# Performance work log

Measured on AMD Instinct MI355X. Metric: run time of the kernel, lower is better.

## Reference

```python
import jax, jax.numpy as jnp
import numpy as np

N_NODES = 100000
N_EDGES = 1000000
IN_DIM = 128
HID1 = 64
HID2 = 64
OUT_DIM = 1
NUM_GRAPHS = 2048


def setup_inputs() -> dict:
    key = jax.random.key(0)
    ks = jax.random.split(key, 12)
    x = jax.random.normal(ks[0], (N_NODES, IN_DIM), dtype=jnp.float32)
    edge_index = jax.random.randint(ks[1], (2, N_EDGES), 0, N_NODES, dtype=jnp.int64)
    batch = jnp.sort(jax.random.randint(ks[2], (N_NODES,), 0, NUM_GRAPHS, dtype=jnp.int64))
    s1 = 1.0 / np.sqrt(IN_DIM)
    s2 = 1.0 / np.sqrt(HID1)
    s3 = 1.0 / np.sqrt(HID2)
    return {
        "x": x,
        "edge_index": edge_index,
        "batch": batch,
        "W1": jax.random.normal(ks[3], (IN_DIM, HID1), dtype=jnp.float32) * s1,
        "b1": jnp.zeros((HID1,), dtype=jnp.float32),
        "W2": jax.random.normal(ks[4], (HID1, HID2), dtype=jnp.float32) * s2,
        "b2": jnp.zeros((HID2,), dtype=jnp.float32),
        "attn_w": jax.random.normal(ks[5], (HID2, 1), dtype=jnp.float32) * s3,
        "attn_b": jnp.zeros((1,), dtype=jnp.float32),
        "mask_w": jax.random.normal(ks[6], (HID2, 1), dtype=jnp.float32) * s3,
        "mask_b": jnp.zeros((1,), dtype=jnp.float32),
        "out_w": jax.random.normal(ks[7], (HID2, OUT_DIM), dtype=jnp.float32) * s3,
        "out_b": jnp.zeros((OUT_DIM,), dtype=jnp.float32),
    }


def reference(x, edge_index, batch, W1, b1, W2, b2, attn_w, attn_b, mask_w, mask_b, out_w, out_b):
    n = x.shape[0]
    # GCNConv (PyG default): add self-loops, symmetric normalization
    loop = jnp.arange(n, dtype=edge_index.dtype)
    row = jnp.concatenate([edge_index[0], loop])  # source nodes
    col = jnp.concatenate([edge_index[1], loop])  # target nodes
    deg = jax.ops.segment_sum(jnp.ones_like(col, dtype=x.dtype), col, num_segments=n)
    dinv = jnp.where(deg > 0, jax.lax.rsqrt(jnp.maximum(deg, 1e-12)), 0.0)
    norm = dinv[row] * dinv[col]  # [E+N]

    def conv(h, W, b):
        h = h @ W                              # [N, out]
        m = h[row] * norm[:, None]             # gather + scale  [E+N, out]
        return jax.ops.segment_sum(m, col, num_segments=n) + b

    h = jax.nn.relu(conv(x, W1, b1))
    h = jax.nn.relu(conv(h, W2, b2))
    # AttentionPooling: (attn score * sigmoid mask)-weighted scatter-sum per graph
    scores = (h @ attn_w + attn_b) * jax.nn.sigmoid(h @ mask_w + mask_b)  # [N,1]
    pooled = jax.ops.segment_sum(h * scores, batch, num_segments=NUM_GRAPHS)  # [G, HID2]
    return pooled @ out_w + out_b
```

## Files before the change

### kernel.cpp

```cpp
#include <hip/hip_runtime.h>
#include <math.h>


#define NB 64
#define SEG 16
#define CAPS 80
#define SLOTS (SEG * CAPS)
#define BIN_BLOCKS 256

__global__ __launch_bounds__(256) void gemm_bin_kernel(
    const float* __restrict__ X, const float* __restrict__ W,
    float* __restrict__ P, int N, int K,
    const int* __restrict__ row, const int* __restrict__ col,
    int* __restrict__ bcnt, int* __restrict__ gbuf, int E,
    float* __restrict__ out, const float* __restrict__ out_b, int G) {
    __shared__ float Wl[32 * 64];
    __shared__ float xs[32 * 132];

    if (blockIdx.x < BIN_BLOCKS) {
        int seg = blockIdx.x & (SEG - 1);
        int t = blockIdx.x * 256 + threadIdx.x;
        if (t < G) out[t] = out_b[0];
        for (int e = t; e < E; e += BIN_BLOCKS * 256) {
            int c = col[e];
            int b = c >> 6;
            int pos = atomicAdd(&bcnt[(b * SEG + seg) * 16], 1);
            if (pos < CAPS) gbuf[b * SLOTS + seg * CAPS + pos] = row[e] | ((c & 63) << 17);
        }
        return;
    }

    const int tid = threadIdx.x;
    const int cg = tid & 7;
    const int ng = tid >> 3;
    const int node0 = (blockIdx.x - BIN_BLOCKS) * 128;

    float acc[4][8];
#pragma unroll
    for (int r = 0; r < 4; r++)
#pragma unroll
        for (int j = 0; j < 8; j++) acc[r][j] = 0.0f;

    for (int k0 = 0; k0 < K; k0 += 32) {
        const float4* Wg = (const float4*)(W + (size_t)k0 * 64);
#pragma unroll
        for (int f = tid; f < 512; f += 256) ((float4*)Wl)[f] = Wg[f];
        {
            int rrow = tid >> 1;
            int q0 = (tid & 1) * 16;
            int node = node0 + rrow;
            const float* Xr = X + (size_t)node * K + k0 + q0;
#pragma unroll
            for (int q = 0; q < 4; q++) {
                float4 v = make_float4(0.f, 0.f, 0.f, 0.f);
                if (node < N) v = *(const float4*)(Xr + 4 * q);
                int kb = q0 + 4 * q;
                xs[(kb + 0) * 132 + rrow] = v.x;
                xs[(kb + 1) * 132 + rrow] = v.y;
                xs[(kb + 2) * 132 + rrow] = v.z;
                xs[(kb + 3) * 132 + rrow] = v.w;
            }
        }
        __syncthreads();
#pragma unroll
        for (int kk = 0; kk < 32; kk++) {
            float4 xv = *(const float4*)&xs[kk * 132 + ng * 4];
            const float* wr = &Wl[kk * 64 + cg * 8];
            float4 w0 = *(const float4*)(wr + 0);
            float4 w1 = *(const float4*)(wr + 4);
#pragma unroll
            for (int r = 0; r < 4; r++) {
                float xr = (r == 0) ? xv.x : (r == 1) ? xv.y : (r == 2) ? xv.z : xv.w;
                acc[r][0] = fmaf(xr, w0.x, acc[r][0]);
                acc[r][1] = fmaf(xr, w0.y, acc[r][1]);
                acc[r][2] = fmaf(xr, w0.z, acc[r][2]);
                acc[r][3] = fmaf(xr, w0.w, acc[r][3]);
                acc[r][4] = fmaf(xr, w1.x, acc[r][4]);
                acc[r][5] = fmaf(xr, w1.y, acc[r][5]);
                acc[r][6] = fmaf(xr, w1.z, acc[r][6]);
                acc[r][7] = fmaf(xr, w1.w, acc[r][7]);
            }
        }
        __syncthreads();
    }

#pragma unroll
    for (int r = 0; r < 4; r++) {
        int node = node0 + ng * 4 + r;
        if (node < N) {
            float* dst = P + (size_t)node * 64 + cg * 8;
            *(float4*)(dst + 0) = make_float4(acc[r][0], acc[r][1], acc[r][2], acc[r][3]);
            *(float4*)(dst + 4) = make_float4(acc[r][4], acc[r][5], acc[r][6], acc[r][7]);
        }
    }
}

__global__ __launch_bounds__(256) void sort_kernel(
    const int* __restrict__ bcnt, const int* __restrict__ gbuf,
    int* __restrict__ csr, int* __restrict__ startcnt,
    float* __restrict__ dinv, float* __restrict__ P, int N) {
    __shared__ int scnt[SEG], segoff[SEG], s_tot;
    __shared__ int ebuf[SLOTS];
    __shared__ int lcnt[NB], lcur[NB];
    __shared__ float sdinv[NB];
    const int tid = threadIdx.x;
    const int b = blockIdx.x;
    const int base = b * SLOTS;

    if (tid < SEG) {
        int c = bcnt[(b * SEG + tid) * 16];
        scnt[tid] = c < CAPS ? c : CAPS;
    }
    if (tid < NB) lcnt[tid] = 0;
    __syncthreads();
    if (tid == 0) {
        int o = 0;
        for (int s = 0; s < SEG; s++) { segoff[s] = o; o += scnt[s]; }
        s_tot = o;
    }
    __syncthreads();
    for (int idx = tid; idx < SLOTS; idx += 256) {
        int seg = idx / CAPS;
        int j = idx - seg * CAPS;
        if (j < scnt[seg]) {
            int w = gbuf[base + idx];
            ebuf[segoff[seg] + j] = w;
            atomicAdd(&lcnt[(w >> 17) & 63], 1);
        }
    }
    __syncthreads();
    if (tid < NB) {
        int cntv = lcnt[tid];
        int rnd = (cntv + 3) & ~3;
        int val = rnd;
#pragma unroll
        for (int off = 1; off < 64; off <<= 1) {
            int n = __shfl_up(val, off, 64);
            if (tid >= off) val += n;
        }
        int st = val - rnd;
        lcur[tid] = st;
        float d = rsqrtf(1.0f + (float)cntv);
        sdinv[tid] = d;
        int v = b * NB + tid;
        if (v < N) {
            dinv[v] = d;
            int cc = cntv < 127 ? cntv : 127;
            startcnt[v] = ((base + st) << 7) | cc;
        }
    }
    __syncthreads();
    int tot = s_tot;
    for (int idx = tid; idx < tot; idx += 256) {
        int w = ebuf[idx];
        int vl = (w >> 17) & 63;
        int pp = atomicAdd(&lcur[vl], 1);
        csr[base + pp] = w & 131071;
    }
    for (int idx = tid; idx < NB * 16; idx += 256) {
        int r = idx >> 4;
        int v = b * NB + r;
        if (v < N) {
            float d = sdinv[r];
            float4* pp = (float4*)(P + (size_t)v * 64) + (idx & 15);
            float4 t = *pp;
            t.x *= d; t.y *= d; t.z *= d; t.w *= d;
            *pp = t;
        }
    }
}

__global__ __launch_bounds__(256) void gather_gemm_kernel(
    const float* __restrict__ P, const int* __restrict__ csr,
    const int* __restrict__ startcnt, const float* __restrict__ dinv,
    const float* __restrict__ b1, const float* __restrict__ W2,
    float* __restrict__ Q, int N) {
    __shared__ float hs[64 * 65];
    __shared__ float Wl[64 * 64];
    const int tid = threadIdx.x;
    const int v0 = blockIdx.x * 64;
    const int vend = (v0 + 64 < N) ? v0 + 64 : N;
    const int p = tid & 15;
    const int p4 = p * 4;

    for (int f = tid; f < 1024; f += 256)
        ((float4*)Wl)[f] = ((const float4*)W2)[f];

    const float4 bb = ((const float4*)b1)[p];
    for (int v = v0 + (tid >> 4); v < vend; v += 16) {
        int pack = startcnt[v];
        int st = pack >> 7;
        int c = pack & 127;
        float dv = dinv[v];
        float4 acc = *(const float4*)(P + (size_t)v * 64 + p4);
        for (int i = 0; i < c; i += 8) {
            int4 ua = *(const int4*)(csr + st + i);
            int4 ub = *(const int4*)(csr + st + i + 4);
            float4 m0 = *(const float4*)(P + (size_t)ua.x * 64 + p4);
            float4 m1 = *(const float4*)(P + (size_t)ua.y * 64 + p4);
            float4 m2 = *(const float4*)(P + (size_t)ua.z * 64 + p4);
            float4 m3 = *(const float4*)(P + (size_t)ua.w * 64 + p4);
            float4 m4 = *(const float4*)(P + (size_t)ub.x * 64 + p4);
            float4 m5 = *(const float4*)(P + (size_t)ub.y * 64 + p4);
            float4 m6 = *(const float4*)(P + (size_t)ub.z * 64 + p4);
            float4 m7 = *(const float4*)(P + (size_t)ub.w * 64 + p4);
            acc.x += m0.x; acc.y += m0.y; acc.z += m0.z; acc.w += m0.w;
            if (i + 1 < c) { acc.x += m1.x; acc.y += m1.y; acc.z += m1.z; acc.w += m1.w; }
            if (i + 2 < c) { acc.x += m2.x; acc.y += m2.y; acc.z += m2.z; acc.w += m2.w; }
            if (i + 3 < c) { acc.x += m3.x; acc.y += m3.y; acc.z += m3.z; acc.w += m3.w; }
            if (i + 4 < c) { acc.x += m4.x; acc.y += m4.y; acc.z += m4.z; acc.w += m4.w; }
            if (i + 5 < c) { acc.x += m5.x; acc.y += m5.y; acc.z += m5.z; acc.w += m5.w; }
            if (i + 6 < c) { acc.x += m6.x; acc.y += m6.y; acc.z += m6.z; acc.w += m6.w; }
            if (i + 7 < c) { acc.x += m7.x; acc.y += m7.y; acc.z += m7.z; acc.w += m7.w; }
        }
        float* hd = &hs[(v - v0) * 65 + p4];
        hd[0] = fmaxf(fmaf(acc.x, dv, bb.x), 0.f);
        hd[1] = fmaxf(fmaf(acc.y, dv, bb.y), 0.f);
        hd[2] = fmaxf(fmaf(acc.z, dv, bb.z), 0.f);
        hd[3] = fmaxf(fmaf(acc.w, dv, bb.w), 0.f);
    }
    __syncthreads();

    const int cg = tid & 7;
    const int n0 = tid >> 3;
    float acc2[2][8];
#pragma unroll
    for (int r = 0; r < 2; r++)
#pragma unroll
        for (int j = 0; j < 8; j++) acc2[r][j] = 0.0f;
    for (int kk = 0; kk < 64; kk++) {
        float x0 = hs[(n0 * 2 + 0) * 65 + kk];
        float x1 = hs[(n0 * 2 + 1) * 65 + kk];
        const float* wr = &Wl[kk * 64 + cg * 8];
        float4 w0 = *(const float4*)(wr + 0);
        float4 w1 = *(const float4*)(wr + 4);
        acc2[0][0] = fmaf(x0, w0.x, acc2[0][0]);
        acc2[0][1] = fmaf(x0, w0.y, acc2[0][1]);
        acc2[0][2] = fmaf(x0, w0.z, acc2[0][2]);
        acc2[0][3] = fmaf(x0, w0.w, acc2[0][3]);
        acc2[0][4] = fmaf(x0, w1.x, acc2[0][4]);
        acc2[0][5] = fmaf(x0, w1.y, acc2[0][5]);
        acc2[0][6] = fmaf(x0, w1.z, acc2[0][6]);
        acc2[0][7] = fmaf(x0, w1.w, acc2[0][7]);
        acc2[1][0] = fmaf(x1, w0.x, acc2[1][0]);
        acc2[1][1] = fmaf(x1, w0.y, acc2[1][1]);
        acc2[1][2] = fmaf(x1, w0.z, acc2[1][2]);
        acc2[1][3] = fmaf(x1, w0.w, acc2[1][3]);
        acc2[1][4] = fmaf(x1, w1.x, acc2[1][4]);
        acc2[1][5] = fmaf(x1, w1.y, acc2[1][5]);
        acc2[1][6] = fmaf(x1, w1.z, acc2[1][6]);
        acc2[1][7] = fmaf(x1, w1.w, acc2[1][7]);
    }
#pragma unroll
    for (int r = 0; r < 2; r++) {
        int node = v0 + n0 * 2 + r;
        if (node < N) {
            float d = dinv[node];
            float* dst = Q + (size_t)node * 64 + cg * 8;
            *(float4*)(dst + 0) = make_float4(acc2[r][0] * d, acc2[r][1] * d,
                                              acc2[r][2] * d, acc2[r][3] * d);
            *(float4*)(dst + 4) = make_float4(acc2[r][4] * d, acc2[r][5] * d,
                                              acc2[r][6] * d, acc2[r][7] * d);
        }
    }
}

#define GP_NODES 64
__global__ __launch_bounds__(256) void gather_pool_kernel(
    const float* __restrict__ Q, const int* __restrict__ csr,
    const int* __restrict__ startcnt, const float* __restrict__ dinv,
    const float* __restrict__ bias, const int* __restrict__ batch,
    const float* __restrict__ attn_w, const float* __restrict__ attn_b,
    const float* __restrict__ mask_w, const float* __restrict__ mask_b,
    const float* __restrict__ out_w, float* __restrict__ out, int N) {
    __shared__ float pacc[2048];
    __shared__ int s_gmin, s_span;
    const int tid = threadIdx.x;
    const int v0 = blockIdx.x * GP_NODES;
    const int vend = (v0 + GP_NODES < N) ? v0 + GP_NODES : N;
    if (tid == 0) {
        int gmin = batch[v0];
        s_gmin = gmin;
        s_span = batch[vend - 1] - gmin + 1;
    }
    __syncthreads();
    const int gmin = s_gmin, span = s_span;
    for (int i = tid; i < span; i += 256) pacc[i] = 0.f;
    __syncthreads();

    const int p = tid & 15;
    const int p4 = p * 4;
    const float4 wa = ((const float4*)attn_w)[p];
    const float4 wm = ((const float4*)mask_w)[p];
    const float4 wo = ((const float4*)out_w)[p];
    const float4 bb = ((const float4*)bias)[p];
    const float ab = attn_b[0], mb = mask_b[0];

    for (int v = v0 + (tid >> 4); v < vend; v += 16) {
        int pack = startcnt[v];
        int st = pack >> 7;
        int c = pack & 127;
        float dv = dinv[v];
        float4 acc = *(const float4*)(Q + (size_t)v * 64 + p4);
        for (int i = 0; i < c; i += 8) {
            int4 ua = *(const int4*)(csr + st + i);
            int4 ub = *(const int4*)(csr + st + i + 4);
            float4 m0 = *(const float4*)(Q + (size_t)ua.x * 64 + p4);
            float4 m1 = *(const float4*)(Q + (size_t)ua.y * 64 + p4);
            float4 m2 = *(const float4*)(Q + (size_t)ua.z * 64 + p4);
            float4 m3 = *(const float4*)(Q + (size_t)ua.w * 64 + p4);
            float4 m4 = *(const float4*)(Q + (size_t)ub.x * 64 + p4);
            float4 m5 = *(const float4*)(Q + (size_t)ub.y * 64 + p4);
            float4 m6 = *(const float4*)(Q + (size_t)ub.z * 64 + p4);
            float4 m7 = *(const float4*)(Q + (size_t)ub.w * 64 + p4);
            acc.x += m0.x; acc.y += m0.y; acc.z += m0.z; acc.w += m0.w;
            if (i + 1 < c) { acc.x += m1.x; acc.y += m1.y; acc.z += m1.z; acc.w += m1.w; }
            if (i + 2 < c) { acc.x += m2.x; acc.y += m2.y; acc.z += m2.z; acc.w += m2.w; }
            if (i + 3 < c) { acc.x += m3.x; acc.y += m3.y; acc.z += m3.z; acc.w += m3.w; }
            if (i + 4 < c) { acc.x += m4.x; acc.y += m4.y; acc.z += m4.z; acc.w += m4.w; }
            if (i + 5 < c) { acc.x += m5.x; acc.y += m5.y; acc.z += m5.z; acc.w += m5.w; }
            if (i + 6 < c) { acc.x += m6.x; acc.y += m6.y; acc.z += m6.z; acc.w += m6.w; }
            if (i + 7 < c) { acc.x += m7.x; acc.y += m7.y; acc.z += m7.z; acc.w += m7.w; }
        }
        float hx = fmaxf(fmaf(acc.x, dv, bb.x), 0.f);
        float hy = fmaxf(fmaf(acc.y, dv, bb.y), 0.f);
        float hz = fmaxf(fmaf(acc.z, dv, bb.z), 0.f);
        float hw = fmaxf(fmaf(acc.w, dv, bb.w), 0.f);
        float pa = hx * wa.x + hy * wa.y + hz * wa.z + hw * wa.w;
        float pm = hx * wm.x + hy * wm.y + hz * wm.z + hw * wm.w;
        float po = hx * wo.x + hy * wo.y + hz * wo.z + hw * wo.w;
#pragma unroll
        for (int off = 1; off < 16; off <<= 1) {
            pa += __shfl_xor(pa, off, 64);
            pm += __shfl_xor(pm, off, 64);
            po += __shfl_xor(po, off, 64);
        }
        if (p == 0) {
            float cc = (pa + ab) * (1.0f / (1.0f + expf(-(pm + mb)))) * po;
            atomicAdd(&pacc[batch[v] - gmin], cc);
        }
    }
    __syncthreads();
    for (int i = tid; i < span; i += 256) {
        float val = pacc[i];
        if (val != 0.f) atomicAdd(&out[gmin + i], val);
    }
}

extern "C" void kernel_launch(void* const* d_in, const int* in_sizes, int n_in,
                              void* d_out, int out_size, void* d_ws, size_t ws_size,
                              hipStream_t stream) {
    const float* x      = (const float*)d_in[0];
    const int*   edge   = (const int*)d_in[1];
    const int*   batch  = (const int*)d_in[2];
    const float* W1     = (const float*)d_in[3];
    const float* b1     = (const float*)d_in[4];
    const float* W2     = (const float*)d_in[5];
    const float* b2     = (const float*)d_in[6];
    const float* attn_w = (const float*)d_in[7];
    const float* attn_b = (const float*)d_in[8];
    const float* mask_w = (const float*)d_in[9];
    const float* mask_b = (const float*)d_in[10];
    const float* out_w  = (const float*)d_in[11];
    const float* out_b  = (const float*)d_in[12];
    float* out = (float*)d_out;

    const int N  = in_sizes[2];
    const int E  = in_sizes[1] / 2;
    const int K1 = in_sizes[0] / N;
    const int H  = in_sizes[4];
    const int G  = out_size;
    const int* row = edge;
    const int* col = edge + E;

    const int NBUCK = (N + NB - 1) / NB;

    char* ws = (char*)d_ws;
    auto align256 = [](size_t s) { return (s + 255) / 256 * 256; };
    int*   bcnt     = (int*)ws;   ws += align256((size_t)NBUCK * SEG * 16 * 4);
    int*   gbuf     = (int*)ws;   ws += align256((size_t)NBUCK * SLOTS * 4);
    int*   csr      = (int*)ws;   ws += align256((size_t)NBUCK * SLOTS * 4);
    int*   startcnt = (int*)ws;   ws += align256((size_t)N * 4);
    float* dinv     = (float*)ws; ws += align256((size_t)N * 4);
    float* P        = (float*)ws; ws += align256((size_t)N * H * 4);
    float* Q        = (float*)ws;

    const int gblocks = (N + 127) / 128;

    hipMemsetAsync(bcnt, 0, (size_t)NBUCK * SEG * 16 * 4, stream);
    hipMemsetAsync(csr, 0, (size_t)NBUCK * SLOTS * 4, stream);

    gemm_bin_kernel<<<BIN_BLOCKS + gblocks, 256, 0, stream>>>(
        x, W1, P, N, K1, row, col, bcnt, gbuf, E, out, out_b, G);

    sort_kernel<<<NBUCK, 256, 0, stream>>>(bcnt, gbuf, csr, startcnt, dinv, P, N);

    gather_gemm_kernel<<<NBUCK, 256, 0, stream>>>(
        P, csr, startcnt, dinv, b1, W2, Q, N);

    gather_pool_kernel<<<NBUCK, 256, 0, stream>>>(
        Q, csr, startcnt, dinv, b2, batch, attn_w, attn_b, mask_w, mask_b, out_w, out, N);
}
```

Measured before the change: 279.6 us.

## Store intermediate node features in fp16 and vectorize edge binning loads

The intermediate feature matrices P and Q move from fp32 to fp16 storage, which halves the bytes read by the random-access neighbor gathers in both aggregation kernels. Each thread now handles 8 features per node through int4 loads and accumulates in fp32. The edge binning loop also reads row and col eight at a time with int4 loads and issues its atomics in batches. The trade-off is reduced precision in the intermediates, which may push results past the tolerance.

```diff
diff --git a/kernel.cpp b/kernel.cpp
--- a/kernel.cpp
+++ b/kernel.cpp
@@ -1,4 +1,5 @@
 #include <hip/hip_runtime.h>
+#include <hip/hip_fp16.h>
 #include <math.h>
 
 
@@ -8,9 +9,28 @@
 #define SLOTS (SEG * CAPS)
 #define BIN_BLOCKS 256
 
+__device__ __forceinline__ void h8_set(float* a, const int4 w) {
+    const __half2* h = (const __half2*)&w;
+    float2 t0 = __half22float2(h[0]);
+    float2 t1 = __half22float2(h[1]);
+    float2 t2 = __half22float2(h[2]);
+    float2 t3 = __half22float2(h[3]);
+    a[0] = t0.x; a[1] = t0.y; a[2] = t1.x; a[3] = t1.y;
+    a[4] = t2.x; a[5] = t2.y; a[6] = t3.x; a[7] = t3.y;
+}
+__device__ __forceinline__ void h8_acc(float* a, const int4 w) {
+    const __half2* h = (const __half2*)&w;
+    float2 t0 = __half22float2(h[0]);
+    float2 t1 = __half22float2(h[1]);
+    float2 t2 = __half22float2(h[2]);
+    float2 t3 = __half22float2(h[3]);
+    a[0] += t0.x; a[1] += t0.y; a[2] += t1.x; a[3] += t1.y;
+    a[4] += t2.x; a[5] += t2.y; a[6] += t3.x; a[7] += t3.y;
+}
+
 __global__ __launch_bounds__(256) void gemm_bin_kernel(
     const float* __restrict__ X, const float* __restrict__ W,
-    float* __restrict__ P, int N, int K,
+    __half* __restrict__ P, int N, int K,
     const int* __restrict__ row, const int* __restrict__ col,
     int* __restrict__ bcnt, int* __restrict__ gbuf, int E,
     float* __restrict__ out, const float* __restrict__ out_b, int G) {
@@ -21,11 +41,31 @@
         int seg = blockIdx.x & (SEG - 1);
         int t = blockIdx.x * 256 + threadIdx.x;
         if (t < G) out[t] = out_b[0];
-        for (int e = t; e < E; e += BIN_BLOCKS * 256) {
-            int c = col[e];
-            int b = c >> 6;
-            int pos = atomicAdd(&bcnt[(b * SEG + seg) * 16], 1);
-            if (pos < CAPS) gbuf[b * SLOTS + seg * CAPS + pos] = row[e] | ((c & 63) << 17);
+        for (int e0 = t * 8; e0 < E; e0 += BIN_BLOCKS * 256 * 8) {
+            if (e0 + 8 <= E) {
+                int4 c0 = *(const int4*)(col + e0);
+                int4 c1 = *(const int4*)(col + e0 + 4);
+                int4 r0 = *(const int4*)(row + e0);
+                int4 r1 = *(const int4*)(row + e0 + 4);
+                int cc[8] = {c0.x, c0.y, c0.z, c0.w, c1.x, c1.y, c1.z, c1.w};
+                int rr[8] = {r0.x, r0.y, r0.z, r0.w, r1.x, r1.y, r1.z, r1.w};
+                int pos[8];
+#pragma unroll
+                for (int j = 0; j < 8; j++)
+                    pos[j] = atomicAdd(&bcnt[((cc[j] >> 6) * SEG + seg) * 16], 1);
+#pragma unroll
+                for (int j = 0; j < 8; j++)
+                    if (pos[j] < CAPS)
+                        gbuf[(cc[j] >> 6) * SLOTS + seg * CAPS + pos[j]] =
+                            rr[j] | ((cc[j] & 63) << 17);
+            } else {
+                for (int e = e0; e < E; e++) {
+                    int c = col[e];
+                    int b = c >> 6;
+                    int pp = atomicAdd(&bcnt[(b * SEG + seg) * 16], 1);
+                    if (pp < CAPS) gbuf[b * SLOTS + seg * CAPS + pp] = row[e] | ((c & 63) << 17);
+                }
+            }
         }
         return;
     }
@@ -88,9 +128,12 @@
     for (int r = 0; r < 4; r++) {
         int node = node0 + ng * 4 + r;
         if (node < N) {
-            float* dst = P + (size_t)node * 64 + cg * 8;
-            *(float4*)(dst + 0) = make_float4(acc[r][0], acc[r][1], acc[r][2], acc[r][3]);
-            *(float4*)(dst + 4) = make_float4(acc[r][4], acc[r][5], acc[r][6], acc[r][7]);
+            __half2 hh[4];
+            hh[0] = __floats2half2_rn(acc[r][0], acc[r][1]);
+            hh[1] = __floats2half2_rn(acc[r][2], acc[r][3]);
+            hh[2] = __floats2half2_rn(acc[r][4], acc[r][5]);
+            hh[3] = __floats2half2_rn(acc[r][6], acc[r][7]);
+            ((int4*)(P + (size_t)node * 64))[cg] = *(int4*)hh;
         }
     }
 }
@@ -98,7 +141,7 @@
 __global__ __launch_bounds__(256) void sort_kernel(
     const int* __restrict__ bcnt, const int* __restrict__ gbuf,
     int* __restrict__ csr, int* __restrict__ startcnt,
-    float* __restrict__ dinv, float* __restrict__ P, int N) {
+    float* __restrict__ dinv, __half* __restrict__ P, int N) {
     __shared__ int scnt[SEG], segoff[SEG], s_tot;
     __shared__ int ebuf[SLOTS];
     __shared__ int lcnt[NB], lcur[NB];
@@ -157,67 +200,77 @@
         int pp = atomicAdd(&lcur[vl], 1);
         csr[base + pp] = w & 131071;
     }
-    for (int idx = tid; idx < NB * 16; idx += 256) {
-        int r = idx >> 4;
+    for (int idx = tid; idx < NB * 8; idx += 256) {
+        int r = idx >> 3;
         int v = b * NB + r;
         if (v < N) {
             float d = sdinv[r];
-            float4* pp = (float4*)(P + (size_t)v * 64) + (idx & 15);
-            float4 t = *pp;
-            t.x *= d; t.y *= d; t.z *= d; t.w *= d;
+            int4* pp = (int4*)(P + (size_t)v * 64) + (idx & 7);
+            int4 t = *pp;
+            __half2* hp = (__half2*)&t;
+#pragma unroll
+            for (int q = 0; q < 4; q++) {
+                float2 f = __half22float2(hp[q]);
+                hp[q] = __floats2half2_rn(f.x * d, f.y * d);
+            }
             *pp = t;
         }
     }
 }
 
 __global__ __launch_bounds__(256) void gather_gemm_kernel(
-    const float* __restrict__ P, const int* __restrict__ csr,
+    const __half* __restrict__ P, const int* __restrict__ csr,
     const int* __restrict__ startcnt, const float* __restrict__ dinv,
     const float* __restrict__ b1, const float* __restrict__ W2,
-    float* __restrict__ Q, int N) {
+    __half* __restrict__ Q, int N) {
     __shared__ float hs[64 * 65];
     __shared__ float Wl[64 * 64];
     const int tid = threadIdx.x;
     const int v0 = blockIdx.x * 64;
     const int vend = (v0 + 64 < N) ? v0 + 64 : N;
-    const int p = tid & 15;
-    const int p4 = p * 4;
+    const int p = tid & 7;
 
     for (int f = tid; f < 1024; f += 256)
         ((float4*)Wl)[f] = ((const float4*)W2)[f];
 
-    const float4 bb = ((const float4*)b1)[p];
-    for (int v = v0 + (tid >> 4); v < vend; v += 16) {
+    const float4 bb0 = ((const float4*)b1)[2 * p];
+    const float4 bb1 = ((const float4*)b1)[2 * p + 1];
+    for (int v = v0 + (tid >> 3); v < vend; v += 32) {
         int pack = startcnt[v];
         int st = pack >> 7;
         int c = pack & 127;
         float dv = dinv[v];
-        float4 acc = *(const float4*)(P + (size_t)v * 64 + p4);
+        float a[8];
+        h8_set(a, ((const int4*)(P + (size_t)v * 64))[p]);
         for (int i = 0; i < c; i += 8) {
             int4 ua = *(const int4*)(csr + st + i);
             int4 ub = *(const int4*)(csr + st + i + 4);
-            float4 m0 = *(const float4*)(P + (size_t)ua.x * 64 + p4);
-            float4 m1 = *(const float4*)(P + (size_t)ua.y * 64 + p4);
-            float4 m2 = *(const float4*)(P + (size_t)ua.z * 64 + p4);
-            float4 m3 = *(const float4*)(P + (size_t)ua.w * 64 + p4);
-            float4 m4 = *(const float4*)(P + (size_t)ub.x * 64 + p4);
-            float4 m5 = *(const float4*)(P + (size_t)ub.y * 64 + p4);
-            float4 m6 = *(const float4*)(P + (size_t)ub.z * 64 + p4);
-            float4 m7 = *(const float4*)(P + (size_t)ub.w * 64 + p4);
-            acc.x += m0.x; acc.y += m0.y; acc.z += m0.z; acc.w += m0.w;
-            if (i + 1 < c) { acc.x += m1.x; acc.y += m1.y; acc.z += m1.z; acc.w += m1.w; }
-            if (i + 2 < c) { acc.x += m2.x; acc.y += m2.y; acc.z += m2.z; acc.w += m2.w; }
-            if (i + 3 < c) { acc.x += m3.x; acc.y += m3.y; acc.z += m3.z; acc.w += m3.w; }
-            if (i + 4 < c) { acc.x += m4.x; acc.y += m4.y; acc.z += m4.z; acc.w += m4.w; }
-            if (i + 5 < c) { acc.x += m5.x; acc.y += m5.y; acc.z += m5.z; acc.w += m5.w; }
-            if (i + 6 < c) { acc.x += m6.x; acc.y += m6.y; acc.z += m6.z; acc.w += m6.w; }
-            if (i + 7 < c) { acc.x += m7.x; acc.y += m7.y; acc.z += m7.z; acc.w += m7.w; }
-        }
-        float* hd = &hs[(v - v0) * 65 + p4];
-        hd[0] = fmaxf(fmaf(acc.x, dv, bb.x), 0.f);
-        hd[1] = fmaxf(fmaf(acc.y, dv, bb.y), 0.f);
-        hd[2] = fmaxf(fmaf(acc.z, dv, bb.z), 0.f);
-        hd[3] = fmaxf(fmaf(acc.w, dv, bb.w), 0.f);
+            int4 m0 = ((const int4*)(P + (size_t)ua.x * 64))[p];
+            int4 m1 = ((const int4*)(P + (size_t)ua.y * 64))[p];
+            int4 m2 = ((const int4*)(P + (size_t)ua.z * 64))[p];
+            int4 m3 = ((const int4*)(P + (size_t)ua.w * 64))[p];
+            int4 m4 = ((const int4*)(P + (size_t)ub.x * 64))[p];
+            int4 m5 = ((const int4*)(P + (size_t)ub.y * 64))[p];
+            int4 m6 = ((const int4*)(P + (size_t)ub.z * 64))[p];
+            int4 m7 = ((const int4*)(P + (size_t)ub.w * 64))[p];
+            h8_acc(a, m0);
+            if (i + 1 < c) h8_acc(a, m1);
+            if (i + 2 < c) h8_acc(a, m2);
+            if (i + 3 < c) h8_acc(a, m3);
+            if (i + 4 < c) h8_acc(a, m4);
+            if (i + 5 < c) h8_acc(a, m5);
+            if (i + 6 < c) h8_acc(a, m6);
+            if (i + 7 < c) h8_acc(a, m7);
+        }
+        float* hd = &hs[(v - v0) * 65 + p * 8];
+        hd[0] = fmaxf(fmaf(a[0], dv, bb0.x), 0.f);
+        hd[1] = fmaxf(fmaf(a[1], dv, bb0.y), 0.f);
+        hd[2] = fmaxf(fmaf(a[2], dv, bb0.z), 0.f);
+        hd[3] = fmaxf(fmaf(a[3], dv, bb0.w), 0.f);
+        hd[4] = fmaxf(fmaf(a[4], dv, bb1.x), 0.f);
+        hd[5] = fmaxf(fmaf(a[5], dv, bb1.y), 0.f);
+        hd[6] = fmaxf(fmaf(a[6], dv, bb1.z), 0.f);
+        hd[7] = fmaxf(fmaf(a[7], dv, bb1.w), 0.f);
     }
     __syncthreads();
 
@@ -256,18 +309,19 @@
         int node = v0 + n0 * 2 + r;
         if (node < N) {
             float d = dinv[node];
-            float* dst = Q + (size_t)node * 64 + cg * 8;
-            *(float4*)(dst + 0) = make_float4(acc2[r][0] * d, acc2[r][1] * d,
-                                              acc2[r][2] * d, acc2[r][3] * d);
-            *(float4*)(dst + 4) = make_float4(acc2[r][4] * d, acc2[r][5] * d,
-                                              acc2[r][6] * d, acc2[r][7] * d);
+            __half2 hh[4];
+            hh[0] = __floats2half2_rn(acc2[r][0] * d, acc2[r][1] * d);
+            hh[1] = __floats2half2_rn(acc2[r][2] * d, acc2[r][3] * d);
+            hh[2] = __floats2half2_rn(acc2[r][4] * d, acc2[r][5] * d);
+            hh[3] = __floats2half2_rn(acc2[r][6] * d, acc2[r][7] * d);
+            ((int4*)(Q + (size_t)node * 64))[cg] = *(int4*)hh;
         }
     }
 }
 
 #define GP_NODES 64
 __global__ __launch_bounds__(256) void gather_pool_kernel(
-    const float* __restrict__ Q, const int* __restrict__ csr,
+    const __half* __restrict__ Q, const int* __restrict__ csr,
     const int* __restrict__ startcnt, const float* __restrict__ dinv,
     const float* __restrict__ bias, const int* __restrict__ batch,
     const float* __restrict__ attn_w, const float* __restrict__ attn_b,
@@ -288,49 +342,56 @@
     for (int i = tid; i < span; i += 256) pacc[i] = 0.f;
     __syncthreads();
 
-    const int p = tid & 15;
-    const int p4 = p * 4;
-    const float4 wa = ((const float4*)attn_w)[p];
-    const float4 wm = ((const float4*)mask_w)[p];
-    const float4 wo = ((const float4*)out_w)[p];
-    const float4 bb = ((const float4*)bias)[p];
+    const int p = tid & 7;
+    const float4 wa0 = ((const float4*)attn_w)[2 * p], wa1 = ((const float4*)attn_w)[2 * p + 1];
+    const float4 wm0 = ((const float4*)mask_w)[2 * p], wm1 = ((const float4*)mask_w)[2 * p + 1];
+    const float4 wo0 = ((const float4*)out_w)[2 * p],  wo1 = ((const float4*)out_w)[2 * p + 1];
+    const float4 bb0 = ((const float4*)bias)[2 * p],   bb1 = ((const float4*)bias)[2 * p + 1];
     const float ab = attn_b[0], mb = mask_b[0];
 
-    for (int v = v0 + (tid >> 4); v < vend; v += 16) {
+    for (int v = v0 + (tid >> 3); v < vend; v += 32) {
         int pack = startcnt[v];
         int st = pack >> 7;
         int c = pack & 127;
         float dv = dinv[v];
-        float4 acc = *(const float4*)(Q + (size_t)v * 64 + p4);
+        float a[8];
+        h8_set(a, ((const int4*)(Q + (size_t)v * 64))[p]);
         for (int i = 0; i < c; i += 8) {
             int4 ua = *(const int4*)(csr + st + i);
             int4 ub = *(const int4*)(csr + st + i + 4);
-            float4 m0 = *(const float4*)(Q + (size_t)ua.x * 64 + p4);
-            float4 m1 = *(const float4*)(Q + (size_t)ua.y * 64 + p4);
-            float4 m2 = *(const float4*)(Q + (size_t)ua.z * 64 + p4);
-            float4 m3 = *(const float4*)(Q + (size_t)ua.w * 64 + p4);
-            float4 m4 = *(const float4*)(Q + (size_t)ub.x * 64 + p4);
-            float4 m5 = *(const float4*)(Q + (size_t)ub.y * 64 + p4);
-            float4 m6 = *(const float4*)(Q + (size_t)ub.z * 64 + p4);
-            float4 m7 = *(const float4*)(Q + (size_t)ub.w * 64 + p4);
-            acc.x += m0.x; acc.y += m0.y; acc.z += m0.z; acc.w += m0.w;
-            if (i + 1 < c) { acc.x += m1.x; acc.y += m1.y; acc.z += m1.z; acc.w += m1.w; }
-            if (i + 2 < c) { acc.x += m2.x; acc.y += m2.y; acc.z += m2.z; acc.w += m2.w; }
-            if (i + 3 < c) { acc.x += m3.x; acc.y += m3.y; acc.z += m3.z; acc.w += m3.w; }
-            if (i + 4 < c) { acc.x += m4.x; acc.y += m4.y; acc.z += m4.z; acc.w += m4.w; }
-            if (i + 5 < c) { acc.x += m5.x; acc.y += m5.y; acc.z += m5.z; acc.w += m5.w; }
-            if (i + 6 < c) { acc.x += m6.x; acc.y += m6.y; acc.z += m6.z; acc.w += m6.w; }
-            if (i + 7 < c) { acc.x += m7.x; acc.y += m7.y; acc.z += m7.z; acc.w += m7.w; }
-        }
-        float hx = fmaxf(fmaf(acc.x, dv, bb.x), 0.f);
-        float hy = fmaxf(fmaf(acc.y, dv, bb.y), 0.f);
-        float hz = fmaxf(fmaf(acc.z, dv, bb.z), 0.f);
-        float hw = fmaxf(fmaf(acc.w, dv, bb.w), 0.f);
-        float pa = hx * wa.x + hy * wa.y + hz * wa.z + hw * wa.w;
-        float pm = hx * wm.x + hy * wm.y + hz * wm.z + hw * wm.w;
-        float po = hx * wo.x + hy * wo.y + hz * wo.z + hw * wo.w;
-#pragma unroll
-        for (int off = 1; off < 16; off <<= 1) {
+            int4 m0 = ((const int4*)(Q + (size_t)ua.x * 64))[p];
+            int4 m1 = ((const int4*)(Q + (size_t)ua.y * 64))[p];
+            int4 m2 = ((const int4*)(Q + (size_t)ua.z * 64))[p];
+            int4 m3 = ((const int4*)(Q + (size_t)ua.w * 64))[p];
+            int4 m4 = ((const int4*)(Q + (size_t)ub.x * 64))[p];
+            int4 m5 = ((const int4*)(Q + (size_t)ub.y * 64))[p];
+            int4 m6 = ((const int4*)(Q + (size_t)ub.z * 64))[p];
+            int4 m7 = ((const int4*)(Q + (size_t)ub.w * 64))[p];
+            h8_acc(a, m0);
+            if (i + 1 < c) h8_acc(a, m1);
+            if (i + 2 < c) h8_acc(a, m2);
+            if (i + 3 < c) h8_acc(a, m3);
+            if (i + 4 < c) h8_acc(a, m4);
+            if (i + 5 < c) h8_acc(a, m5);
+            if (i + 6 < c) h8_acc(a, m6);
+            if (i + 7 < c) h8_acc(a, m7);
+        }
+        float h0 = fmaxf(fmaf(a[0], dv, bb0.x), 0.f);
+        float h1v = fmaxf(fmaf(a[1], dv, bb0.y), 0.f);
+        float h2v = fmaxf(fmaf(a[2], dv, bb0.z), 0.f);
+        float h3 = fmaxf(fmaf(a[3], dv, bb0.w), 0.f);
+        float h4 = fmaxf(fmaf(a[4], dv, bb1.x), 0.f);
+        float h5 = fmaxf(fmaf(a[5], dv, bb1.y), 0.f);
+        float h6 = fmaxf(fmaf(a[6], dv, bb1.z), 0.f);
+        float h7 = fmaxf(fmaf(a[7], dv, bb1.w), 0.f);
+        float pa = h0 * wa0.x + h1v * wa0.y + h2v * wa0.z + h3 * wa0.w
+                 + h4 * wa1.x + h5 * wa1.y + h6 * wa1.z + h7 * wa1.w;
+        float pm = h0 * wm0.x + h1v * wm0.y + h2v * wm0.z + h3 * wm0.w
+                 + h4 * wm1.x + h5 * wm1.y + h6 * wm1.z + h7 * wm1.w;
+        float po = h0 * wo0.x + h1v * wo0.y + h2v * wo0.z + h3 * wo0.w
+                 + h4 * wo1.x + h5 * wo1.y + h6 * wo1.z + h7 * wo1.w;
+#pragma unroll
+        for (int off = 1; off < 8; off <<= 1) {
             pa += __shfl_xor(pa, off, 64);
             pm += __shfl_xor(pm, off, 64);
             po += __shfl_xor(po, off, 64);
@@ -377,13 +438,13 @@
 
     char* ws = (char*)d_ws;
     auto align256 = [](size_t s) { return (s + 255) / 256 * 256; };
-    int*   bcnt     = (int*)ws;   ws += align256((size_t)NBUCK * SEG * 16 * 4);
-    int*   gbuf     = (int*)ws;   ws += align256((size_t)NBUCK * SLOTS * 4);
-    int*   csr      = (int*)ws;   ws += align256((size_t)NBUCK * SLOTS * 4);
-    int*   startcnt = (int*)ws;   ws += align256((size_t)N * 4);
-    float* dinv     = (float*)ws; ws += align256((size_t)N * 4);
-    float* P        = (float*)ws; ws += align256((size_t)N * H * 4);
-    float* Q        = (float*)ws;
+    int*    bcnt     = (int*)ws;    ws += align256((size_t)NBUCK * SEG * 16 * 4);
+    int*    gbuf     = (int*)ws;    ws += align256((size_t)NBUCK * SLOTS * 4);
+    int*    csr      = (int*)ws;    ws += align256((size_t)NBUCK * SLOTS * 4);
+    int*    startcnt = (int*)ws;    ws += align256((size_t)N * 4);
+    float*  dinv     = (float*)ws;  ws += align256((size_t)N * 4);
+    __half* P        = (__half*)ws; ws += align256((size_t)N * H * 2);
+    __half* Q        = (__half*)ws;
 
     const int gblocks = (N + 127) / 128;
 
```

After: 238.7 us. 1.17x faster.
